# Kernel optimization log

Measured on AMD Instinct MI355X. Metric: run time of the kernel, lower is better.

## Reference

```python
import jax, jax.numpy as jnp
import numpy as np

B, N, L, C, H = 8, 300, 4096, 256, 8
DH = C // H  # 32; doubled to 64 after concat with pos/sine embeddings


def _linear_params(key, fan_in, fan_out):
    kw, kb = jax.random.split(key)
    bound = 1.0 / np.sqrt(fan_in)
    W = jax.random.uniform(kw, (fan_out, fan_in), jnp.float32, -bound, bound)
    b = jax.random.uniform(kb, (fan_out,), jnp.float32, -bound, bound)
    return W, b


def setup_inputs() -> dict:
    key = jax.random.key(0)
    ks = jax.random.split(key, 13)
    inp = {
        "query": jax.random.normal(ks[0], (B, N, C), jnp.float32),
        "key": jax.random.normal(ks[1], (B, L, C), jnp.float32),
        "value": jax.random.normal(ks[2], (B, L, C), jnp.float32),
        "query_pos": jax.random.normal(ks[3], (B, N, C), jnp.float32),
        "key_pos": jax.random.normal(ks[4], (B, L, C), jnp.float32),
        "query_sine_embed": jax.random.normal(ks[5], (B, N, C), jnp.float32),
    }
    names = ["qc", "qp", "qs", "kc", "kp", "v", "o"]
    for i, nm in enumerate(names):
        W, b = _linear_params(ks[6 + i], C, C)
        inp[f"W{nm}"] = W
        inp[f"b{nm}"] = b
    return inp


def reference(query, key, value, query_pos, key_pos, query_sine_embed,
              Wqc, bqc, Wqp, bqp, Wqs, bqs, Wkc, bkc, Wkp, bkp, Wv, bv, Wo, bo):
    lin = lambda x, W, b: jnp.einsum("bnc,dc->bnd", x, W) + b
    qc = lin(query, Wqc, bqc)                  # (B, N, C)
    kc = lin(key, Wkc, bkc)                    # (B, L, C)
    v = lin(value, Wv, bv)                     # (B, L, C)
    kp = lin(key_pos, Wkp, bkp)                # (B, L, C)
    qp = lin(query_pos, Wqp, bqp)              # is_first=True branch
    q = qc + qp
    k = kc + kp
    qs = lin(query_sine_embed, Wqs, bqs)
    # split heads and concat content with positional/sine embedding -> head dim 2*DH
    q = jnp.concatenate([q.reshape(B, N, H, DH), qs.reshape(B, N, H, DH)], axis=3)   # (B,N,H,2DH)
    k = jnp.concatenate([k.reshape(B, L, H, DH), kp.reshape(B, L, H, DH)], axis=3)   # (B,L,H,2DH)
    vh = v.reshape(B, L, H, DH)
    scale = (2 * DH) ** -0.5
    attn = jnp.einsum("bnhd,blhd->bhnl", q * scale, k)      # (B,H,N,L)
    attn = jax.nn.softmax(attn, axis=-1)
    out = jnp.einsum("bhnl,blhd->bnhd", attn, vh).reshape(B, N, C)
    out = jnp.einsum("bnc,dc->bnd", out, Wo) + bo
    return query + out  # identity = query
```

## Files before the change

kernel.cpp:

```cpp
#include <hip/hip_runtime.h>
#include <hip/hip_bf16.h>

using bf8_t = __attribute__((ext_vector_type(8))) short;
using bf4_t = __attribute__((ext_vector_type(4))) short;
using u16x4 = __attribute__((ext_vector_type(4))) unsigned short;
using f32x4 = __attribute__((ext_vector_type(4))) float;

constexpr int B_   = 8;
constexpr int N_   = 300;
constexpr int L_   = 4096;
constexpr int C_   = 256;
constexpr int H_   = 8;
constexpr int NPAD = 320;
constexpr int QT_  = 5;
constexpr int SPL_ = 4;
constexpr int TPS_ = 16;
constexpr float SCALE = 0.18033688011112042f;

__device__ __forceinline__ unsigned short f2b(float f) {
  unsigned u = __float_as_uint(f);
  u += 0x7FFFu + ((u >> 16) & 1u);
  return (unsigned short)(u >> 16);
}

__device__ __forceinline__ void stage_cvt16(unsigned short* dst, const float* src) {
#pragma unroll
  for (int half = 0; half < 2; ++half) {
    f32x4 x0 = *(const f32x4*)(src + half * 8);
    f32x4 x1 = *(const f32x4*)(src + half * 8 + 4);
    bf8_t v;
#pragma unroll
    for (int j = 0; j < 4; ++j) { v[j] = (short)f2b(x0[j]); v[4 + j] = (short)f2b(x1[j]); }
    *(bf8_t*)(dst + half * 8) = v;
  }
}

__device__ __forceinline__ void gload_lds16(const void* g, void* l) {
  __builtin_amdgcn_global_load_lds(
      (const __attribute__((address_space(1))) unsigned int*)g,
      (__attribute__((address_space(3))) unsigned int*)l, 16, 0, 0);
}

__device__ __forceinline__ unsigned cvt_pk_bf16(float lo, float hi) {
  unsigned r;
  asm("v_cvt_pk_bf16_f32 %0, %1, %2" : "=v"(r) : "v"(lo), "v"(hi));
  return r;
}

__global__ __launch_bounds__(256) void wcvt_all_k(
    const float* __restrict__ W0, const float* __restrict__ W1, const float* __restrict__ W2,
    const float* __restrict__ W3, const float* __restrict__ W4, const float* __restrict__ W5,
    unsigned short* __restrict__ Wk, unsigned short* __restrict__ Wq)
{
  const float* Wkv[3] = {W0, W1, W2};
  const float* Wqq[3] = {W3, W4, W5};
  const int x = blockIdx.x, i = blockIdx.y;
  const int d = threadIdx.x;
  {
    const float* src = Wkv[i] + (size_t)d * C_ + x * 32;
    unsigned short* dst = Wk + ((size_t)(i * 8 + x) * 256 + d) * 32;
#pragma unroll
    for (int g = 0; g < 4; ++g) {
      f32x4 a = *(const f32x4*)(src + g * 8);
      f32x4 b = *(const f32x4*)(src + g * 8 + 4);
      bf8_t v;
#pragma unroll
      for (int j = 0; j < 4; ++j) { v[j] = (short)f2b(a[j]); v[4 + j] = (short)f2b(b[j]); }
      *(bf8_t*)(dst + (g ^ (d & 3)) * 8) = v;
    }
  }
  if (x < 4) {
    const float* src = Wqq[i] + (size_t)d * C_ + x * 64;
    unsigned short* dst = Wq + ((size_t)(i * 4 + x) * 256 + d) * 64;
#pragma unroll
    for (int g = 0; g < 8; ++g) {
      f32x4 a = *(const f32x4*)(src + g * 8);
      f32x4 b = *(const f32x4*)(src + g * 8 + 4);
      bf8_t v;
#pragma unroll
      for (int j = 0; j < 4; ++j) { v[j] = (short)f2b(a[j]); v[4 + j] = (short)f2b(b[j]); }
      *(bf8_t*)(dst + (g ^ (d & 7)) * 8) = v;
    }
  }
}

__global__ __launch_bounds__(256, 4) void kvproj_k(
    const float* __restrict__ xp, const float* __restrict__ xk, const float* __restrict__ xv,
    const unsigned short* __restrict__ Wk,
    const float* __restrict__ bkp, const float* __restrict__ bkc, const float* __restrict__ bv,
    unsigned short* __restrict__ Kc, unsigned short* __restrict__ Kp, unsigned short* __restrict__ Vt)
{
  __shared__ __align__(16) unsigned short LB[20480];
  const int tid = threadIdx.x, lane = tid & 63, wv = tid >> 6;
  const int fr = lane & 15, fg = lane >> 4;
  const int i = blockIdx.y;
  const int row0 = blockIdx.x * 64;
  const int b = row0 >> 12, ll0 = row0 & (L_ - 1);
  const float* X    = (i == 0) ? xp  : (i == 1) ? xk  : xv;
  const float* bias = (i == 0) ? bkp : (i == 1) ? bkc : bv;

  const int ar = tid >> 2, ac = tid & 3;
  const int agx = (ac ^ (ar & 3)) * 8;

  f32x4 acc[4][4] = {};

  const unsigned short* Wi = Wk + (size_t)i * 8 * 8192;

  auto stageB = [&](int step, int buf) {
    const char* src = (const char*)(Wi + step * 8192);
    char* dst = (char*)(LB + 4096 + buf * 8192);
#pragma unroll
    for (int c = 0; c < 4; ++c) {
      const int off = c * 4096 + tid * 16;
      gload_lds16(src + off, dst + off);
    }
  };
  auto stageA_load = [&](int step, f32x4* arg) {
    const float* s = X + (size_t)(row0 + ar) * C_ + step * 32 + ac * 8;
    arg[0] = *(const f32x4*)s;
    arg[1] = *(const f32x4*)(s + 4);
  };
  auto stageA_write = [&](int buf, const f32x4* arg) {
    bf8_t v;
#pragma unroll
    for (int j = 0; j < 4; ++j) { v[j] = (short)f2b(arg[0][j]); v[4 + j] = (short)f2b(arg[1][j]); }
    *(bf8_t*)(LB + buf * 2048 + ar * 32 + agx) = v;
  };

  {
    f32x4 a0[2];
    stageA_load(0, a0);
    stageB(0, 0);
    stageA_write(0, a0);
  }
  __syncthreads();

  int cur = 0;
  const int gx = (fg ^ (fr & 3)) * 8;
  for (int step = 0; step < 8; ++step) {
    const int nxt = cur ^ 1;
    f32x4 arn[2];
    if (step < 7) {
      stageA_load(step + 1, arn);
      stageB(step + 1, nxt);
    }
    const unsigned short* Ab = LB + cur * 2048;
    const unsigned short* Bb = LB + 4096 + cur * 8192;
    bf8_t xf[4];
#pragma unroll
    for (int mt = 0; mt < 4; ++mt)
      xf[mt] = *(const bf8_t*)(Ab + (mt * 16 + fr) * 32 + gx);
#pragma unroll
    for (int nt = 0; nt < 4; ++nt) {
      bf8_t wf = *(const bf8_t*)(Bb + (wv * 64 + nt * 16 + fr) * 32 + gx);
#pragma unroll
      for (int mt = 0; mt < 4; ++mt)
        acc[nt][mt] = __builtin_amdgcn_mfma_f32_16x16x32_bf16(wf, xf[mt], acc[nt][mt], 0, 0, 0);
    }
    if (step < 7) stageA_write(nxt, arn);
    __syncthreads();
    cur = nxt;
  }

  if (i < 2) {
    unsigned short* outp = (i == 0) ? Kp : Kc;
#pragma unroll
    for (int nt = 0; nt < 4; ++nt) {
      const int d0 = wv * 64 + nt * 16 + fg * 4;
      const f32x4 bb = *(const f32x4*)(bias + d0);
      const int h = d0 >> 5, dh = d0 & 31;
#pragma unroll
      for (int mt = 0; mt < 4; ++mt) {
        const int l = ll0 + mt * 16 + fr;
        u16x4 v;
#pragma unroll
        for (int r = 0; r < 4; ++r) v[r] = f2b(acc[nt][mt][r] + bb[r]);
        *(u16x4*)(outp + ((size_t)(b * H_ + h) * L_ + l) * 32 + dh) = v;
      }
    }
  } else {
    unsigned short* T = LB;
#pragma unroll
    for (int nt = 0; nt < 4; ++nt) {
      const int d0 = wv * 64 + nt * 16 + fg * 4;
      const f32x4 bb = *(const f32x4*)(bias + d0);
#pragma unroll
      for (int mt = 0; mt < 4; ++mt)
#pragma unroll
        for (int r = 0; r < 4; ++r)
          T[(d0 + r) * 68 + mt * 16 + fr] = f2b(acc[nt][mt][r] + bb[r]);
    }
    __syncthreads();
    const int d = tid;
    unsigned short* dst = Vt + ((size_t)(b * H_ + (d >> 5)) * 32 + (d & 31)) * L_ + ll0;
#pragma unroll
    for (int j = 0; j < 16; ++j)
      *(u16x4*)(dst + j * 4) = *(const u16x4*)(T + d * 68 + j * 4);
  }
}

__global__ __launch_bounds__(256, 2) void qproj_k(
    const float* __restrict__ xp, const float* __restrict__ xq, const float* __restrict__ xs,
    const unsigned short* __restrict__ Wq,
    const float* __restrict__ bqp, const float* __restrict__ bqc, const float* __restrict__ bqs,
    unsigned short* __restrict__ Qcat)
{
  __shared__ __align__(16) unsigned short Al[2][64 * 64];
  __shared__ __align__(16) unsigned short Bl[2][256 * 64];
  const int tid = threadIdx.x, lane = tid & 63, wv = tid >> 6;
  const int fr = lane & 15, fg = lane >> 4;
  const int b = blockIdx.x / 5, n0 = (blockIdx.x % 5) * 64;
  const float* Ax[3] = {xp, xq, xs};

  const int sr = tid >> 2, sc = (tid & 3) * 16;
  const int ag = sc >> 3;
  const bool arow_ok = (n0 + sr) < N_;

  f32x4 acc[16] = {};

  auto stageB = [&](int step, int buf) {
    const char* bsrc = (const char*)Wq + (size_t)step * 32768;
    char* bdst = (char*)&Bl[buf][0];
#pragma unroll
    for (int c = 0; c < 8; ++c) {
      const int off = c * 4096 + wv * 1024 + lane * 16;
      gload_lds16(bsrc + off, bdst + off);
    }
  };
  auto stageA_load = [&](int step, f32x4* ar) {
    const int i = step >> 2, kt = step & 3;
    if (arow_ok) {
      const float* src = Ax[i] + ((size_t)b * N_ + n0 + sr) * C_ + kt * 64 + sc;
#pragma unroll
      for (int j = 0; j < 4; ++j) ar[j] = *(const f32x4*)(src + j * 4);
    } else {
#pragma unroll
      for (int j = 0; j < 4; ++j) ar[j] = (f32x4){0.f, 0.f, 0.f, 0.f};
    }
  };
  auto stageA_write = [&](int buf, const f32x4* ar) {
    unsigned short* base = &Al[buf][sr * 64];
    bf8_t v0, v1;
#pragma unroll
    for (int j = 0; j < 4; ++j) {
      v0[j] = (short)f2b(ar[0][j]); v0[4 + j] = (short)f2b(ar[1][j]);
      v1[j] = (short)f2b(ar[2][j]); v1[4 + j] = (short)f2b(ar[3][j]);
    }
    *(bf8_t*)(base + ((ag ^ (sr & 7)) * 8))       = v0;
    *(bf8_t*)(base + (((ag | 1) ^ (sr & 7)) * 8)) = v1;
  };

  {
    f32x4 a0[4];
    stageA_load(0, a0);
    stageB(0, 0);
    stageA_write(0, a0);
  }
  __syncthreads();

  int cur = 0;
  const int xrow = wv * 16 + fr;
  const int n_out = n0 + wv * 16 + fr;
  const bool ok = n_out < N_;
  for (int step = 0; step < 12; ++step) {
    const int nxt = cur ^ 1;
    f32x4 arn[4];
    if (step < 11) {
      stageA_load(step + 1, arn);
      stageB(step + 1, nxt);
    }
    const unsigned short* Ab = &Al[cur][0];
    const unsigned short* Bb = &Bl[cur][0];
#pragma unroll
    for (int kh = 0; kh < 2; ++kh) {
      const int gxx = (4 * kh + fg) ^ (fr & 7);
      bf8_t xf = *(const bf8_t*)(Ab + xrow * 64 + gxx * 8);
#pragma unroll
      for (int nt = 0; nt < 16; ++nt) {
        bf8_t wf = *(const bf8_t*)(Bb + (nt * 16 + fr) * 64 + gxx * 8);
        acc[nt] = __builtin_amdgcn_mfma_f32_16x16x32_bf16(wf, xf, acc[nt], 0, 0, 0);
      }
    }
    if (step == 7 || step == 11) {
      const int off = (step == 7) ? 0 : 32;
#pragma unroll
      for (int nt = 0; nt < 16; ++nt) {
        const int d0 = nt * 16 + fg * 4;
        f32x4 bb = *(const f32x4*)(bqp + d0) + *(const f32x4*)(bqc + d0);
        if (step == 11) bb += *(const f32x4*)(bqs + d0);
        u16x4 v;
#pragma unroll
        for (int r = 0; r < 4; ++r) v[r] = ok ? f2b((acc[nt][r] + bb[r]) * SCALE) : (unsigned short)0;
        *(u16x4*)(Qcat + ((size_t)(b * H_ + (d0 >> 5)) * NPAD + n_out) * 64 + off + (d0 & 31)) = v;
      }
    }
    if (step < 11) stageA_write(nxt, arn);
    __syncthreads();
    cur = nxt;
  }
}

__global__ __launch_bounds__(256, 5) void attn_k(
    const unsigned short* __restrict__ Qcat, const unsigned short* __restrict__ Kc,
    const unsigned short* __restrict__ Kp, const unsigned short* __restrict__ Vt,
    float* __restrict__ PO, float* __restrict__ PM, float* __restrict__ PLs)
{
  __shared__ __align__(16) unsigned short Kcl[2][64 * 36];
  __shared__ __align__(16) unsigned short Kpl[2][64 * 36];
  __shared__ __align__(16) unsigned short Vp[2][32][72];
  const int x = blockIdx.x;
  const int qt = x >> 8;
  const int rem = x & 255;
  const int s = rem & (SPL_ - 1);
  const int h = (rem >> 2) & (H_ - 1);
  const int b = rem >> 5;
  const int n0 = qt * 64;
  const int tid = threadIdx.x, lane = tid & 63, wv = tid >> 6;
  const int fr = lane & 15, fg = lane >> 4;

  const unsigned short* Qb = Qcat + ((size_t)b * H_ + h) * NPAD * 64;
  bf8_t qf[2];
  {
    const int qrow = n0 + wv * 16 + fr;
    qf[0] = *(const bf8_t*)&Qb[(size_t)qrow * 64 + 8 * fg];
    qf[1] = *(const bf8_t*)&Qb[(size_t)qrow * 64 + 32 + 8 * fg];
  }
  float m_r = -1e30f, l_r = 0.f;
  f32x4 o[2] = {};

  const unsigned short* KcB = Kc + ((size_t)b * H_ + h) * L_ * 32;
  const unsigned short* KpB = Kp + ((size_t)b * H_ + h) * L_ * 32;
  const unsigned short* VB  = Vt + ((size_t)b * H_ + h) * 32 * (size_t)L_;

  const int sl = tid >> 2, sg = tid & 3;
  const int vd = tid >> 3, vc = (tid & 7) * 8;

  auto loadK = [&](int t, bf8_t* kc2, bf8_t* kp2) {
    const size_t off = ((size_t)(t * 64 + sl)) * 32 + sg * 8;
    *kc2 = *(const bf8_t*)(KcB + off);
    *kp2 = *(const bf8_t*)(KpB + off);
  };

  const int t0 = s * TPS_, t1 = t0 + TPS_;
  bf8_t kcr, kpr, vreg;
  loadK(t0, &kcr, &kpr);
  vreg = *(const bf8_t*)(VB + (size_t)vd * L_ + t0 * 64 + vc);

  int cur = 0;
  for (int t = t0; t < t1; ++t) {
    {
      unsigned short* kd = &Kcl[cur][sl * 36 + sg * 8];
      unsigned short* pd = &Kpl[cur][sl * 36 + sg * 8];
      bf4_t lo, hi;
#pragma unroll
      for (int j = 0; j < 4; ++j) { lo[j] = kcr[j]; hi[j] = kcr[4 + j]; }
      *(bf4_t*)kd = lo; *(bf4_t*)(kd + 4) = hi;
#pragma unroll
      for (int j = 0; j < 4; ++j) { lo[j] = kpr[j]; hi[j] = kpr[4 + j]; }
      *(bf4_t*)pd = lo; *(bf4_t*)(pd + 4) = hi;
      *(bf8_t*)&Vp[cur][vd][vc] = vreg;
    }
    __syncthreads();
    if (t + 1 < t1) {
      loadK(t + 1, &kcr, &kpr);
      vreg = *(const bf8_t*)(VB + (size_t)vd * L_ + (t + 1) * 64 + vc);
    }
    f32x4 sc[4] = {};
#pragma unroll
    for (int nf = 0; nf < 4; ++nf) {
      const unsigned short* pc = &Kcl[cur][(nf * 16 + fr) * 36 + 8 * fg];
      const unsigned short* pp = &Kpl[cur][(nf * 16 + fr) * 36 + 8 * fg];
      bf4_t c0 = *(const bf4_t*)pc, c1 = *(const bf4_t*)(pc + 4);
      bf4_t p0 = *(const bf4_t*)pp, p1 = *(const bf4_t*)(pp + 4);
      bf8_t kf0, kf1;
#pragma unroll
      for (int j = 0; j < 4; ++j) {
        kf0[j] = c0[j]; kf0[4 + j] = c1[j];
        kf1[j] = p0[j]; kf1[4 + j] = p1[j];
      }
      sc[nf] = __builtin_amdgcn_mfma_f32_16x16x32_bf16(kf0, qf[0], sc[nf], 0, 0, 0);
      sc[nf] = __builtin_amdgcn_mfma_f32_16x16x32_bf16(kf1, qf[1], sc[nf], 0, 0, 0);
    }
    float mx = fmaxf(fmaxf(sc[0][0], sc[0][1]), fmaxf(sc[0][2], sc[0][3]));
#pragma unroll
    for (int nf = 1; nf < 4; ++nf)
      mx = fmaxf(mx, fmaxf(fmaxf(sc[nf][0], sc[nf][1]), fmaxf(sc[nf][2], sc[nf][3])));
    mx = fmaxf(mx, __shfl_xor(mx, 16));
    mx = fmaxf(mx, __shfl_xor(mx, 32));
    if (!__all(mx <= m_r + 8.f)) {
      const float mnew = fmaxf(m_r, mx);
      const float corr = exp2f(m_r - mnew);
      l_r *= corr;
#pragma unroll
      for (int r = 0; r < 4; ++r) { o[0][r] *= corr; o[1][r] *= corr; }
      m_r = mnew;
    }
    float ps = 0.f;
#pragma unroll
    for (int nf = 0; nf < 4; ++nf)
#pragma unroll
      for (int r = 0; r < 4; ++r) {
        const float p = exp2f(sc[nf][r] - m_r);
        sc[nf][r] = p;
        ps += p;
      }
    ps += __shfl_xor(ps, 16);
    ps += __shfl_xor(ps, 32);
    l_r += ps;
    unsigned pw[8];
#pragma unroll
    for (int nf = 0; nf < 4; ++nf) {
      pw[2 * nf]     = cvt_pk_bf16(sc[nf][0], sc[nf][1]);
      pw[2 * nf + 1] = cvt_pk_bf16(sc[nf][2], sc[nf][3]);
    }
#pragma unroll
    for (int kh = 0; kh < 2; ++kh) {
      union { unsigned u[4]; bf8_t v; } pu;
      pu.u[0] = pw[4 * kh];     pu.u[1] = pw[4 * kh + 1];
      pu.u[2] = pw[4 * kh + 2]; pu.u[3] = pw[4 * kh + 3];
      const bf8_t pf = pu.v;
#pragma unroll
      for (int df = 0; df < 2; ++df) {
        const unsigned short* vrow = &Vp[cur][df * 16 + fr][0];
        bf4_t va = *(const bf4_t*)(vrow + kh * 32 + fg * 4);
        bf4_t vb = *(const bf4_t*)(vrow + kh * 32 + 16 + fg * 4);
        bf8_t vf;
#pragma unroll
        for (int j = 0; j < 4; ++j) { vf[j] = va[j]; vf[4 + j] = vb[j]; }
        o[df] = __builtin_amdgcn_mfma_f32_16x16x32_bf16(vf, pf, o[df], 0, 0, 0);
      }
    }
    cur ^= 1;
  }
  const int rec = (((b * H_) + h) * QT_ + qt) * SPL_ + s;
  const int q = wv * 16 + fr;
  if (fg == 0) {
    PM [rec * 64 + q] = m_r;
    PLs[rec * 64 + q] = l_r;
  }
#pragma unroll
  for (int df = 0; df < 2; ++df)
    *(f32x4*)(PO + ((size_t)rec * 64 + q) * 32 + df * 16 + fg * 4) = o[df];
}

__global__ __launch_bounds__(256) void combine_k(
    const float* __restrict__ PO, const float* __restrict__ PM, const float* __restrict__ PLs,
    unsigned short* __restrict__ aout)
{
  const int qt = blockIdx.x, h = blockIdx.y, b = blockIdx.z;
  const int tid = threadIdx.x;
  const int row = tid >> 2, dh0 = (tid & 3) * 8;
  const int rec0 = (((b * H_) + h) * QT_ + qt) * SPL_;
  float m[SPL_], w[SPL_];
  float M = -1e30f;
#pragma unroll
  for (int s = 0; s < SPL_; ++s) { m[s] = PM[(rec0 + s) * 64 + row]; M = fmaxf(M, m[s]); }
  float denom = 0.f;
#pragma unroll
  for (int s = 0; s < SPL_; ++s) {
    w[s] = exp2f(m[s] - M);
    denom += w[s] * PLs[(rec0 + s) * 64 + row];
  }
  float num[8] = {};
#pragma unroll
  for (int s = 0; s < SPL_; ++s) {
    const float* po = PO + ((size_t)(rec0 + s) * 64 + row) * 32 + dh0;
    f32x4 a = *(const f32x4*)po;
    f32x4 c = *(const f32x4*)(po + 4);
#pragma unroll
    for (int j = 0; j < 4; ++j) { num[j] += w[s] * a[j]; num[4 + j] += w[s] * c[j]; }
  }
  const int n = qt * 64 + row;
  if (n < N_) {
    const float inv = 1.f / denom;
    bf8_t v;
#pragma unroll
    for (int j = 0; j < 8; ++j) v[j] = (short)f2b(num[j] * inv);
    *(bf8_t*)(aout + ((size_t)b * NPAD + n) * C_ + h * 32 + dh0) = v;
  }
}

__global__ __launch_bounds__(256) void oproj_k(
    const unsigned short* __restrict__ aout, const float* __restrict__ Wo,
    const float* __restrict__ bo, const float* __restrict__ query,
    float* __restrict__ out)
{
  __shared__ __align__(16) unsigned short Al[64][72];
  __shared__ __align__(16) unsigned short Bl[64][72];
  const int b = blockIdx.z, n0 = blockIdx.y * 64, d0 = blockIdx.x * 64;
  const int tid = threadIdx.x, lane = tid & 63, wv = tid >> 6;
  const int wm = wv >> 1, wn = wv & 1;
  const int sr = tid >> 2, sc = (tid & 3) * 16;
  const int fr = lane & 15, fg = lane >> 4;
  f32x4 acc[2][2] = {};

  for (int kt = 0; kt < 4; ++kt) {
    const int k0 = kt * 64;
    {
      const unsigned short* src = aout + ((size_t)b * NPAD + n0 + sr) * C_ + k0 + sc;
      *(bf8_t*)&Al[sr][sc]     = *(const bf8_t*)src;
      *(bf8_t*)&Al[sr][sc + 8] = *(const bf8_t*)(src + 8);
    }
    stage_cvt16(&Bl[sr][sc], Wo + (size_t)(d0 + sr) * C_ + k0 + sc);
    __syncthreads();
#pragma unroll
    for (int kh = 0; kh < 2; ++kh) {
      const int ko = kh * 32 + 8 * fg;
      bf8_t af[2], bq[2];
#pragma unroll
      for (int m = 0; m < 2; ++m) {
        af[m] = *(const bf8_t*)&Al[wm * 32 + m * 16 + fr][ko];
        bq[m] = *(const bf8_t*)&Bl[wn * 32 + m * 16 + fr][ko];
      }
#pragma unroll
      for (int m = 0; m < 2; ++m)
#pragma unroll
        for (int n = 0; n < 2; ++n)
          acc[m][n] = __builtin_amdgcn_mfma_f32_16x16x32_bf16(af[m], bq[n], acc[m][n], 0, 0, 0);
    }
    __syncthreads();
  }
#pragma unroll
  for (int m = 0; m < 2; ++m)
#pragma unroll
    for (int nn = 0; nn < 2; ++nn) {
      const int d = d0 + wn * 32 + nn * 16 + fr;
      const float bb = bo[d];
#pragma unroll
      for (int r = 0; r < 4; ++r) {
        const int n = n0 + wm * 32 + m * 16 + fg * 4 + r;
        if (n < N_) {
          const size_t gi = ((size_t)b * N_ + n) * C_ + d;
          out[gi] = acc[m][nn][r] + bb + query[gi];
        }
      }
    }
}

extern "C" void kernel_launch(void* const* d_in, const int* in_sizes, int n_in,
                              void* d_out, int out_size, void* d_ws, size_t ws_size,
                              hipStream_t stream)
{
  const float* query = (const float*)d_in[0];
  const float* key   = (const float*)d_in[1];
  const float* value = (const float*)d_in[2];
  const float* qpos  = (const float*)d_in[3];
  const float* kpos  = (const float*)d_in[4];
  const float* qsine = (const float*)d_in[5];
  const float* Wqc = (const float*)d_in[6];  const float* bqc = (const float*)d_in[7];
  const float* Wqp = (const float*)d_in[8];  const float* bqp = (const float*)d_in[9];
  const float* Wqs = (const float*)d_in[10]; const float* bqs = (const float*)d_in[11];
  const float* Wkc = (const float*)d_in[12]; const float* bkc = (const float*)d_in[13];
  const float* Wkp = (const float*)d_in[14]; const float* bkp = (const float*)d_in[15];
  const float* Wv  = (const float*)d_in[16]; const float* bv  = (const float*)d_in[17];
  const float* Wo  = (const float*)d_in[18]; const float* bo  = (const float*)d_in[19];

  const size_t qcat_b = (size_t)B_ * H_ * NPAD * 64 * 2;
  const size_t kc_b   = (size_t)B_ * H_ * L_ * 32 * 2;
  const size_t kp_b   = kc_b;
  const size_t vt_b   = kc_b;
  const size_t aout_b = (size_t)B_ * NPAD * C_ * 2;
  const size_t nrec   = (size_t)B_ * H_ * QT_ * SPL_;
  const size_t po_b   = nrec * 64 * 32 * 4;
  const size_t pm_b   = nrec * 64 * 4;
  const size_t pl_b   = nrec * 64 * 4;
  const size_t wsw_b  = (size_t)24 * 256 * 64 * 2;
  if (ws_size < qcat_b + kc_b + kp_b + vt_b + aout_b + po_b + pm_b + pl_b + wsw_b) return;
  char* ws = (char*)d_ws;
  unsigned short* Qcat = (unsigned short*)(ws);
  unsigned short* Kc   = (unsigned short*)(ws + qcat_b);
  unsigned short* Kp   = (unsigned short*)(ws + qcat_b + kc_b);
  unsigned short* Vt   = (unsigned short*)(ws + qcat_b + kc_b + kp_b);
  unsigned short* aout = (unsigned short*)(ws + qcat_b + kc_b + kp_b + vt_b);
  float* PO  = (float*)(ws + qcat_b + kc_b + kp_b + vt_b + aout_b);
  float* PM  = (float*)(ws + qcat_b + kc_b + kp_b + vt_b + aout_b + po_b);
  float* PLs = (float*)(ws + qcat_b + kc_b + kp_b + vt_b + aout_b + po_b + pm_b);
  unsigned short* Wq = (unsigned short*)(ws + qcat_b + kc_b + kp_b + vt_b + aout_b + po_b + pm_b + pl_b);
  unsigned short* Wk = Wq + (size_t)12 * 16384;
  float* out = (float*)d_out;

  wcvt_all_k<<<dim3(8, 3),                256, 0, stream>>>(Wkp, Wkc, Wv, Wqp, Wqc, Wqs, Wk, Wq);
  qproj_k  <<<dim3(B_ * QT_),             256, 0, stream>>>(qpos, query, qsine, Wq, bqp, bqc, bqs, Qcat);
  kvproj_k <<<dim3(512, 3),               256, 0, stream>>>(kpos, key, value, Wk, bkp, bkc, bv, Kc, Kp, Vt);
  attn_k   <<<dim3(QT_ * SPL_ * B_ * H_), 256, 0, stream>>>(Qcat, Kc, Kp, Vt, PO, PM, PLs);
  combine_k<<<dim3(QT_, 8, 8),            256, 0, stream>>>(PO, PM, PLs, aout);
  oproj_k  <<<dim3(4, QT_, 8),            256, 0, stream>>>(aout, Wo, bo, query, out);
}
```

Before: 127.0 us.

## Fuse split-softmax combine into output projection; widen K/V projection blocks

The separate combine kernel is removed. The output projection now merges the four partial softmax results (max, sum, partial output) directly while staging its A tile, which drops one launch and the bf16 round trip through the attention-output buffer. Separately, the K/V projection block grows to 512 threads covering 128 rows, each wave computing 32 output columns by 128 rows, so each weight tile is reused across more rows. The cost is that combine work is repeated for each of the four output-column blocks, and the larger block may lower occupancy.

```diff
diff --git a/kernel.cpp b/kernel.cpp
--- a/kernel.cpp
+++ b/kernel.cpp
@@ -21,18 +21,6 @@
   unsigned u = __float_as_uint(f);
   u += 0x7FFFu + ((u >> 16) & 1u);
   return (unsigned short)(u >> 16);
-}
-
-__device__ __forceinline__ void stage_cvt16(unsigned short* dst, const float* src) {
-#pragma unroll
-  for (int half = 0; half < 2; ++half) {
-    f32x4 x0 = *(const f32x4*)(src + half * 8);
-    f32x4 x1 = *(const f32x4*)(src + half * 8 + 4);
-    bf8_t v;
-#pragma unroll
-    for (int j = 0; j < 4; ++j) { v[j] = (short)f2b(x0[j]); v[4 + j] = (short)f2b(x1[j]); }
-    *(bf8_t*)(dst + half * 8) = v;
-  }
 }
 
 __device__ __forceinline__ void gload_lds16(const void* g, void* l) {
@@ -84,17 +72,17 @@
   }
 }
 
-__global__ __launch_bounds__(256, 4) void kvproj_k(
+__global__ __launch_bounds__(512, 4) void kvproj_k(
     const float* __restrict__ xp, const float* __restrict__ xk, const float* __restrict__ xv,
     const unsigned short* __restrict__ Wk,
     const float* __restrict__ bkp, const float* __restrict__ bkc, const float* __restrict__ bv,
     unsigned short* __restrict__ Kc, unsigned short* __restrict__ Kp, unsigned short* __restrict__ Vt)
 {
-  __shared__ __align__(16) unsigned short LB[20480];
+  __shared__ __align__(16) unsigned short LB[24576];
   const int tid = threadIdx.x, lane = tid & 63, wv = tid >> 6;
   const int fr = lane & 15, fg = lane >> 4;
   const int i = blockIdx.y;
-  const int row0 = blockIdx.x * 64;
+  const int row0 = blockIdx.x * 128;
   const int b = row0 >> 12, ll0 = row0 & (L_ - 1);
   const float* X    = (i == 0) ? xp  : (i == 1) ? xk  : xv;
   const float* bias = (i == 0) ? bkp : (i == 1) ? bkc : bv;
@@ -102,16 +90,16 @@
   const int ar = tid >> 2, ac = tid & 3;
   const int agx = (ac ^ (ar & 3)) * 8;
 
-  f32x4 acc[4][4] = {};
+  f32x4 acc[2][8] = {};
 
   const unsigned short* Wi = Wk + (size_t)i * 8 * 8192;
 
   auto stageB = [&](int step, int buf) {
     const char* src = (const char*)(Wi + step * 8192);
-    char* dst = (char*)(LB + 4096 + buf * 8192);
-#pragma unroll
-    for (int c = 0; c < 4; ++c) {
-      const int off = c * 4096 + tid * 16;
+    char* dst = (char*)(LB + 8192 + buf * 8192);
+#pragma unroll
+    for (int c = 0; c < 2; ++c) {
+      const int off = c * 8192 + tid * 16;
       gload_lds16(src + off, dst + off);
     }
   };
@@ -124,7 +112,7 @@
     bf8_t v;
 #pragma unroll
     for (int j = 0; j < 4; ++j) { v[j] = (short)f2b(arg[0][j]); v[4 + j] = (short)f2b(arg[1][j]); }
-    *(bf8_t*)(LB + buf * 2048 + ar * 32 + agx) = v;
+    *(bf8_t*)(LB + buf * 4096 + ar * 32 + agx) = v;
   };
 
   {
@@ -144,18 +132,17 @@
       stageA_load(step + 1, arn);
       stageB(step + 1, nxt);
     }
-    const unsigned short* Ab = LB + cur * 2048;
-    const unsigned short* Bb = LB + 4096 + cur * 8192;
-    bf8_t xf[4];
-#pragma unroll
-    for (int mt = 0; mt < 4; ++mt)
-      xf[mt] = *(const bf8_t*)(Ab + (mt * 16 + fr) * 32 + gx);
-#pragma unroll
-    for (int nt = 0; nt < 4; ++nt) {
-      bf8_t wf = *(const bf8_t*)(Bb + (wv * 64 + nt * 16 + fr) * 32 + gx);
-#pragma unroll
-      for (int mt = 0; mt < 4; ++mt)
-        acc[nt][mt] = __builtin_amdgcn_mfma_f32_16x16x32_bf16(wf, xf[mt], acc[nt][mt], 0, 0, 0);
+    const unsigned short* Ab = LB + cur * 4096;
+    const unsigned short* Bb = LB + 8192 + cur * 8192;
+    bf8_t wf[2];
+#pragma unroll
+    for (int nt = 0; nt < 2; ++nt)
+      wf[nt] = *(const bf8_t*)(Bb + (wv * 32 + nt * 16 + fr) * 32 + gx);
+#pragma unroll
+    for (int mt = 0; mt < 8; ++mt) {
+      bf8_t xf = *(const bf8_t*)(Ab + (mt * 16 + fr) * 32 + gx);
+      acc[0][mt] = __builtin_amdgcn_mfma_f32_16x16x32_bf16(wf[0], xf, acc[0][mt], 0, 0, 0);
+      acc[1][mt] = __builtin_amdgcn_mfma_f32_16x16x32_bf16(wf[1], xf, acc[1][mt], 0, 0, 0);
     }
     if (step < 7) stageA_write(nxt, arn);
     __syncthreads();
@@ -165,12 +152,12 @@
   if (i < 2) {
     unsigned short* outp = (i == 0) ? Kp : Kc;
 #pragma unroll
-    for (int nt = 0; nt < 4; ++nt) {
-      const int d0 = wv * 64 + nt * 16 + fg * 4;
+    for (int nt = 0; nt < 2; ++nt) {
+      const int d0 = wv * 32 + nt * 16 + fg * 4;
       const f32x4 bb = *(const f32x4*)(bias + d0);
       const int h = d0 >> 5, dh = d0 & 31;
 #pragma unroll
-      for (int mt = 0; mt < 4; ++mt) {
+      for (int mt = 0; mt < 8; ++mt) {
         const int l = ll0 + mt * 16 + fr;
         u16x4 v;
 #pragma unroll
@@ -181,21 +168,28 @@
   } else {
     unsigned short* T = LB;
 #pragma unroll
-    for (int nt = 0; nt < 4; ++nt) {
-      const int d0 = wv * 64 + nt * 16 + fg * 4;
-      const f32x4 bb = *(const f32x4*)(bias + d0);
-#pragma unroll
-      for (int mt = 0; mt < 4; ++mt)
-#pragma unroll
-        for (int r = 0; r < 4; ++r)
-          T[(d0 + r) * 68 + mt * 16 + fr] = f2b(acc[nt][mt][r] + bb[r]);
-    }
-    __syncthreads();
-    const int d = tid;
-    unsigned short* dst = Vt + ((size_t)(b * H_ + (d >> 5)) * 32 + (d & 31)) * L_ + ll0;
-#pragma unroll
-    for (int j = 0; j < 16; ++j)
-      *(u16x4*)(dst + j * 4) = *(const u16x4*)(T + d * 68 + j * 4);
+    for (int half = 0; half < 2; ++half) {
+#pragma unroll
+      for (int nt = 0; nt < 2; ++nt) {
+        const int d0 = wv * 32 + nt * 16 + fg * 4;
+        const f32x4 bb = *(const f32x4*)(bias + d0);
+#pragma unroll
+        for (int m2 = 0; m2 < 4; ++m2) {
+          const int mt = half * 4 + m2;
+#pragma unroll
+          for (int r = 0; r < 4; ++r)
+            T[(d0 + r) * 68 + m2 * 16 + fr] = f2b(acc[nt][mt][r] + bb[r]);
+        }
+      }
+      __syncthreads();
+      const int d = tid >> 1, lh = (tid & 1) * 32;
+      unsigned short* dst = Vt + ((size_t)(b * H_ + (d >> 5)) * 32 + (d & 31)) * L_
+                               + ll0 + half * 64 + lh;
+#pragma unroll
+      for (int j = 0; j < 8; ++j)
+        *(u16x4*)(dst + j * 4) = *(const u16x4*)(T + d * 68 + lh + j * 4);
+      __syncthreads();
+    }
   }
 }
 
@@ -443,51 +437,15 @@
     *(f32x4*)(PO + ((size_t)rec * 64 + q) * 32 + df * 16 + fg * 4) = o[df];
 }
 
-__global__ __launch_bounds__(256) void combine_k(
+__global__ __launch_bounds__(256) void oproj_k(
     const float* __restrict__ PO, const float* __restrict__ PM, const float* __restrict__ PLs,
-    unsigned short* __restrict__ aout)
-{
-  const int qt = blockIdx.x, h = blockIdx.y, b = blockIdx.z;
-  const int tid = threadIdx.x;
-  const int row = tid >> 2, dh0 = (tid & 3) * 8;
-  const int rec0 = (((b * H_) + h) * QT_ + qt) * SPL_;
-  float m[SPL_], w[SPL_];
-  float M = -1e30f;
-#pragma unroll
-  for (int s = 0; s < SPL_; ++s) { m[s] = PM[(rec0 + s) * 64 + row]; M = fmaxf(M, m[s]); }
-  float denom = 0.f;
-#pragma unroll
-  for (int s = 0; s < SPL_; ++s) {
-    w[s] = exp2f(m[s] - M);
-    denom += w[s] * PLs[(rec0 + s) * 64 + row];
-  }
-  float num[8] = {};
-#pragma unroll
-  for (int s = 0; s < SPL_; ++s) {
-    const float* po = PO + ((size_t)(rec0 + s) * 64 + row) * 32 + dh0;
-    f32x4 a = *(const f32x4*)po;
-    f32x4 c = *(const f32x4*)(po + 4);
-#pragma unroll
-    for (int j = 0; j < 4; ++j) { num[j] += w[s] * a[j]; num[4 + j] += w[s] * c[j]; }
-  }
-  const int n = qt * 64 + row;
-  if (n < N_) {
-    const float inv = 1.f / denom;
-    bf8_t v;
-#pragma unroll
-    for (int j = 0; j < 8; ++j) v[j] = (short)f2b(num[j] * inv);
-    *(bf8_t*)(aout + ((size_t)b * NPAD + n) * C_ + h * 32 + dh0) = v;
-  }
-}
-
-__global__ __launch_bounds__(256) void oproj_k(
-    const unsigned short* __restrict__ aout, const float* __restrict__ Wo,
-    const float* __restrict__ bo, const float* __restrict__ query,
-    float* __restrict__ out)
+    const float* __restrict__ Wo, const float* __restrict__ bo,
+    const float* __restrict__ query, float* __restrict__ out)
 {
   __shared__ __align__(16) unsigned short Al[64][72];
   __shared__ __align__(16) unsigned short Bl[64][72];
-  const int b = blockIdx.z, n0 = blockIdx.y * 64, d0 = blockIdx.x * 64;
+  const int b = blockIdx.z, qt = blockIdx.y, d0 = blockIdx.x * 64;
+  const int n0 = qt * 64;
   const int tid = threadIdx.x, lane = tid & 63, wv = tid >> 6;
   const int wm = wv >> 1, wn = wv & 1;
   const int sr = tid >> 2, sc = (tid & 3) * 16;
@@ -497,11 +455,54 @@
   for (int kt = 0; kt < 4; ++kt) {
     const int k0 = kt * 64;
     {
-      const unsigned short* src = aout + ((size_t)b * NPAD + n0 + sr) * C_ + k0 + sc;
-      *(bf8_t*)&Al[sr][sc]     = *(const bf8_t*)src;
-      *(bf8_t*)&Al[sr][sc + 8] = *(const bf8_t*)(src + 8);
-    }
-    stage_cvt16(&Bl[sr][sc], Wo + (size_t)(d0 + sr) * C_ + k0 + sc);
+      const int kk = k0 + sc;
+      const int h = kk >> 5, dh0 = kk & 31;
+      const int rec0 = (((b * H_) + h) * QT_ + qt) * SPL_;
+      float mm[SPL_], w4[SPL_];
+      float M = -1e30f;
+#pragma unroll
+      for (int s = 0; s < SPL_; ++s) { mm[s] = PM[(rec0 + s) * 64 + sr]; M = fmaxf(M, mm[s]); }
+      float denom = 0.f;
+#pragma unroll
+      for (int s = 0; s < SPL_; ++s) {
+        w4[s] = exp2f(mm[s] - M);
+        denom += w4[s] * PLs[(rec0 + s) * 64 + sr];
+      }
+      f32x4 num[4] = {};
+#pragma unroll
+      for (int s = 0; s < SPL_; ++s) {
+        const float* po = PO + ((size_t)(rec0 + s) * 64 + sr) * 32 + dh0;
+#pragma unroll
+        for (int j4 = 0; j4 < 4; ++j4) {
+          f32x4 p = *(const f32x4*)(po + j4 * 4);
+#pragma unroll
+          for (int e = 0; e < 4; ++e) num[j4][e] += w4[s] * p[e];
+        }
+      }
+      const float inv = 1.f / denom;
+#pragma unroll
+      for (int hlf = 0; hlf < 2; ++hlf) {
+        bf8_t v;
+#pragma unroll
+        for (int e = 0; e < 4; ++e) {
+          v[e]     = (short)f2b(num[2 * hlf][e] * inv);
+          v[4 + e] = (short)f2b(num[2 * hlf + 1][e] * inv);
+        }
+        *(bf8_t*)(&Al[sr][sc] + hlf * 8) = v;
+      }
+    }
+    {
+      const float* src = Wo + (size_t)(d0 + sr) * C_ + k0 + sc;
+#pragma unroll
+      for (int half = 0; half < 2; ++half) {
+        f32x4 x0 = *(const f32x4*)(src + half * 8);
+        f32x4 x1 = *(const f32x4*)(src + half * 8 + 4);
+        bf8_t v;
+#pragma unroll
+        for (int j = 0; j < 4; ++j) { v[j] = (short)f2b(x0[j]); v[4 + j] = (short)f2b(x1[j]); }
+        *(bf8_t*)(&Bl[sr][sc] + half * 8) = v;
+      }
+    }
     __syncthreads();
 #pragma unroll
     for (int kh = 0; kh < 2; ++kh) {
@@ -571,7 +572,6 @@
   unsigned short* Kc   = (unsigned short*)(ws + qcat_b);
   unsigned short* Kp   = (unsigned short*)(ws + qcat_b + kc_b);
   unsigned short* Vt   = (unsigned short*)(ws + qcat_b + kc_b + kp_b);
-  unsigned short* aout = (unsigned short*)(ws + qcat_b + kc_b + kp_b + vt_b);
   float* PO  = (float*)(ws + qcat_b + kc_b + kp_b + vt_b + aout_b);
   float* PM  = (float*)(ws + qcat_b + kc_b + kp_b + vt_b + aout_b + po_b);
   float* PLs = (float*)(ws + qcat_b + kc_b + kp_b + vt_b + aout_b + po_b + pm_b);
@@ -581,8 +581,7 @@
 
   wcvt_all_k<<<dim3(8, 3),                256, 0, stream>>>(Wkp, Wkc, Wv, Wqp, Wqc, Wqs, Wk, Wq);
   qproj_k  <<<dim3(B_ * QT_),             256, 0, stream>>>(qpos, query, qsine, Wq, bqp, bqc, bqs, Qcat);
-  kvproj_k <<<dim3(512, 3),               256, 0, stream>>>(kpos, key, value, Wk, bkp, bkc, bv, Kc, Kp, Vt);
+  kvproj_k <<<dim3(256, 3),               512, 0, stream>>>(kpos, key, value, Wk, bkp, bkc, bv, Kc, Kp, Vt);
   attn_k   <<<dim3(QT_ * SPL_ * B_ * H_), 256, 0, stream>>>(Qcat, Kc, Kp, Vt, PO, PM, PLs);
-  combine_k<<<dim3(QT_, 8, 8),            256, 0, stream>>>(PO, PM, PLs, aout);
-  oproj_k  <<<dim3(4, QT_, 8),            256, 0, stream>>>(aout, Wo, bo, query, out);
-}
+  oproj_k  <<<dim3(4, QT_, 8),            256, 0, stream>>>(PO, PM, PLs, Wo, bo, query, out);
+}
```

Result: slower. 130.4 us (+2.7%).
